# Kernel optimization log

Hardware: AMD Instinct MI355X
Metric: run time of the kernel (lower is better)

## Reference

```python
import jax, jax.numpy as jnp
import numpy as np

KERNEL = 31
GROUPS = 8
EPS = 1e-5


def mha1d(x, Wq, Wk, Wv, rel):
    """Sliding-window multi-head attention (MutliHeadAttention1D).
    x: [b, s, in_f]; Wq/Wk/Wv: [out_f, in_f] (torch Linear layout); rel: [1, out_f, KERNEL].
    Returns (out [b, s, out_f], attn [b, s, GROUPS, KERNEL])."""
    b, s, _ = x.shape
    out_f = Wq.shape[0]
    d = out_f // GROUPS
    pad = (KERNEL - 1) // 2
    xp = jnp.pad(x, ((0, 0), (pad, pad), (0, 0)))
    q = jnp.einsum('bsf,of->bso', x, Wq)          # [b, s, out_f]
    k = jnp.einsum('bsf,of->bso', xp, Wk)         # [b, s+2*pad, out_f]
    v = jnp.einsum('bsf,of->bso', xp, Wv)
    # unfold: window index [s, KERNEL]
    idx = jnp.arange(s)[:, None] + jnp.arange(KERNEL)[None, :]
    kw = jnp.swapaxes(k[:, idx], 2, 3) + rel       # [b, s, out_f, KERNEL]
    vw = jnp.swapaxes(v[:, idx], 2, 3)             # [b, s, out_f, KERNEL]
    kw = kw.reshape(b, s, GROUPS, d, KERNEL)
    vw = vw.reshape(b, s, GROUPS, d, KERNEL)
    qh = q.reshape(b, s, GROUPS, d, 1)
    energy = jnp.sum(qh * kw, axis=-2, keepdims=True)   # [b, s, g, 1, K]
    attn = jax.nn.softmax(energy, axis=-1)               # [b, s, g, 1, K]
    out = jnp.sum(attn * vw, axis=-1).reshape(b, s, out_f)
    return out, attn[:, :, :, 0, :]


def layer_norm(x, g, b):
    mu = jnp.mean(x, axis=-1, keepdims=True)
    var = jnp.mean(jnp.square(x - mu), axis=-1, keepdims=True)
    return (x - mu) / jnp.sqrt(var + EPS) * g + b


def setup_inputs() -> dict:
    key = jax.random.key(0)
    ks = jax.random.split(key, 20)
    in_f, mc, out_f = 229, 48, 88
    d = {}
    d['spec'] = jax.random.normal(ks[0], (8, 8192, in_f), dtype=jnp.float32)
    # onset attention block (in 229 -> 48)
    d['Wq1'] = jax.random.normal(ks[1], (mc, in_f), dtype=jnp.float32) * 0.1
    d['Wk1'] = jax.random.normal(ks[2], (mc, in_f), dtype=jnp.float32) * 0.1
    d['Wv1'] = jax.random.normal(ks[3], (mc, in_f), dtype=jnp.float32) * 0.1
    d['rel1'] = jax.random.normal(ks[4], (1, mc, KERNEL), dtype=jnp.float32)
    d['ln1_g'] = jnp.ones((mc,), jnp.float32)
    d['ln1_b'] = jnp.zeros((mc,), jnp.float32)
    d['Wo'] = jax.random.normal(ks[5], (out_f, mc), dtype=jnp.float32) * 0.1
    d['bo'] = jnp.zeros((out_f,), jnp.float32)
    # frame attention block (in 48+88=136 -> 48)
    in2 = mc + out_f
    d['Wq2'] = jax.random.normal(ks[6], (mc, in2), dtype=jnp.float32) * 0.1
    d['Wk2'] = jax.random.normal(ks[7], (mc, in2), dtype=jnp.float32) * 0.1
    d['Wv2'] = jax.random.normal(ks[8], (mc, in2), dtype=jnp.float32) * 0.1
    d['rel2'] = jax.random.normal(ks[9], (1, mc, KERNEL), dtype=jnp.float32)
    d['ln2_g'] = jnp.ones((mc,), jnp.float32)
    d['ln2_b'] = jnp.zeros((mc,), jnp.float32)
    d['Wf'] = jax.random.normal(ks[10], (out_f, mc), dtype=jnp.float32) * 0.1
    d['bf'] = jnp.zeros((out_f,), jnp.float32)
    return d


def reference(spec, Wq1, Wk1, Wv1, rel1, ln1_g, ln1_b, Wo, bo,
              Wq2, Wk2, Wv2, rel2, ln2_g, ln2_b, Wf, bf):
    x, a = mha1d(spec, Wq1, Wk1, Wv1, rel1)
    x = layer_norm(x, ln1_g, ln1_b)
    onset_pred = jax.nn.sigmoid(jnp.einsum('bsm,om->bso', x, Wo) + bo)
    x = jnp.concatenate((onset_pred, x), axis=-1)
    x, _ = mha1d(x, Wq2, Wk2, Wv2, rel2)
    x = layer_norm(x, ln2_g, ln2_b)
    frame_pred = jax.nn.sigmoid(jnp.einsum('bsm,om->bso', x, Wf) + bf)
    return frame_pred, onset_pred, a
```

## Files before the change

kernel.cpp:

```cpp
#include <hip/hip_runtime.h>
#include <math.h>

namespace {

constexpr int B_   = 8;
constexpr int S_   = 8192;
constexpr int NROW = B_ * S_;
constexpr int MC   = 48;
constexpr int OF   = 88;
constexpr int KW   = 31;
constexpr int F1   = 229;
constexpr int F2   = 136;

typedef __attribute__((ext_vector_type(8))) short bf16x8;
typedef __attribute__((ext_vector_type(4))) float f32x4;

__device__ inline unsigned short f2bf(float v) {
    unsigned u = __float_as_uint(v);
    unsigned r = (u + 0x7FFFu + ((u >> 16) & 1u)) >> 16;
    return (unsigned short)r;
}
__device__ inline float bf2f(unsigned short b) {
    return __uint_as_float((unsigned)b << 16);
}
__device__ inline unsigned pack2(unsigned short a, unsigned short b) {
    return (unsigned)a | ((unsigned)b << 16);
}

__global__ void wprep_kernel(const float* __restrict__ Wq,
                             const float* __restrict__ Wk,
                             const float* __restrict__ Wv,
                             int K, int nch, unsigned short* __restrict__ out) {
    int idx = blockIdx.x * 256 + threadIdx.x;
    int kpad = nch * 32;
    int total = 144 * kpad;
    if (idx >= total) return;
    int oc = idx / kpad;
    int kg = idx - oc * kpad;
    int c  = kg >> 5, kk = kg & 31;
    float val = 0.f;
    if (kg < K) {
        const float* W = (oc < 48) ? Wq : (oc < 96 ? Wk : Wv);
        int ocl = (oc < 48) ? oc : (oc < 96 ? oc - 48 : oc - 96);
        val = W[ocl * K + kg];
    }
    unsigned short h = f2bf(val);
    unsigned short l = f2bf(val - bf2f(h));
    size_t base = (size_t)c * 16384 + (size_t)oc * 56 + kk;
    out[base]        = h;
    out[base + 8192] = l;
}

__global__ void woprep_kernel(const float* __restrict__ W,
                              unsigned short* __restrict__ out) {
    int idx = blockIdx.x * 256 + threadIdx.x;
    if (idx >= 96 * 64) return;
    int n = idx >> 6, k = idx & 63;
    float val = (n < OF && k < MC) ? W[n * MC + k] : 0.f;
    unsigned short h = f2bf(val);
    unsigned short l = f2bf(val - bf2f(h));
    out[idx]        = h;
    out[6144 + idx] = l;
}

template<int K, int NCH>
__global__ __launch_bounds__(256) void proj_mfma(
    const float* __restrict__ x,
    const unsigned short* __restrict__ wbuf,
    float* __restrict__ qo, float* __restrict__ ko, float* __restrict__ vo)
{
    __shared__ __attribute__((aligned(16))) unsigned short Ah[64 * 56];
    __shared__ __attribute__((aligned(16))) unsigned short Al[64 * 56];
    __shared__ __attribute__((aligned(16))) unsigned short Bblk[16384];

    const int tid  = threadIdx.x;
    const int row0 = blockIdx.x * 64;
    const int lane = tid & 63;
    const int wm   = tid >> 6;

    f32x4 acc[9];
    #pragma unroll
    for (int nt = 0; nt < 9; ++nt) acc[nt] = f32x4{0.f, 0.f, 0.f, 0.f};

    const int arow = wm * 16 + (lane & 15);
    const int ak   = (lane >> 4) * 8;

    for (int c = 0; c < NCH; ++c) {
        {
            const uint4* src = (const uint4*)(wbuf + (size_t)c * 16384);
            uint4* dst = (uint4*)Bblk;
            #pragma unroll
            for (int i = 0; i < 8; ++i)
                dst[tid + 256 * i] = src[tid + 256 * i];
        }
        const int kc = c * 32;
        #pragma unroll
        for (int i = 0; i < 4; ++i) {
            int idx = tid + 256 * i;
            int r   = idx >> 4;
            int k2  = (idx & 15) * 2;
            int kg  = kc + k2;
            const float* xr = x + (size_t)(row0 + r) * K;
            float v0 = (kg     < K) ? xr[kg]     : 0.f;
            float v1 = (kg + 1 < K) ? xr[kg + 1] : 0.f;
            unsigned short h0 = f2bf(v0), h1 = f2bf(v1);
            unsigned short l0 = f2bf(v0 - bf2f(h0));
            unsigned short l1 = f2bf(v1 - bf2f(h1));
            *(unsigned*)&Ah[r * 56 + k2] = pack2(h0, h1);
            *(unsigned*)&Al[r * 56 + k2] = pack2(l0, l1);
        }
        __syncthreads();

        bf16x8 ah = *(const bf16x8*)&Ah[arow * 56 + ak];
        bf16x8 al = *(const bf16x8*)&Al[arow * 56 + ak];
        #pragma unroll
        for (int nt = 0; nt < 9; ++nt) {
            int bcol = nt * 16 + (lane & 15);
            bf16x8 bh = *(const bf16x8*)&Bblk[bcol * 56 + ak];
            bf16x8 bl = *(const bf16x8*)&Bblk[8192 + bcol * 56 + ak];
            acc[nt] = __builtin_amdgcn_mfma_f32_16x16x32_bf16(ah, bh, acc[nt], 0, 0, 0);
            acc[nt] = __builtin_amdgcn_mfma_f32_16x16x32_bf16(ah, bl, acc[nt], 0, 0, 0);
            acc[nt] = __builtin_amdgcn_mfma_f32_16x16x32_bf16(al, bh, acc[nt], 0, 0, 0);
        }
        __syncthreads();
    }

    const int orow = row0 + wm * 16 + ((lane >> 4) << 2);
    const int ocol = lane & 15;
    #pragma unroll
    for (int nt = 0; nt < 9; ++nt) {
        float* dst = (nt < 3) ? qo : (nt < 6 ? ko : vo);
        int oc = (nt % 3) * 16 + ocol;
        #pragma unroll
        for (int rg = 0; rg < 4; ++rg)
            dst[(size_t)(orow + rg) * MC + oc] = acc[nt][rg];
    }
}

template<bool FIRST>
__global__ __launch_bounds__(256, 4) void attn_kernel(
    const float* __restrict__ qb,
    const float* __restrict__ kb,
    const float* __restrict__ vb,
    const float* __restrict__ rel,
    const float* __restrict__ lng,
    const float* __restrict__ lnb,
    const unsigned short* __restrict__ wop,
    const float* __restrict__ bo,
    float* __restrict__ pred,
    float* __restrict__ attn_out,
    float* __restrict__ x2)
{
    __shared__ __attribute__((aligned(16))) float ks[62 * 52];
    __shared__ __attribute__((aligned(16))) float vs[62 * 52];
    __shared__ __attribute__((aligned(16))) float relT[31 * 52];
    __shared__ __attribute__((aligned(16))) unsigned short lnbuf[2][32 * 48 + 64];
    __shared__ float bosL[96];
    __shared__ float lngs[48], lnbs[48];

    const int tid  = threadIdx.x;
    const int bb   = blockIdx.x >> 8;
    const int st0  = (blockIdx.x & 255) * 32;
    const size_t base = (size_t)bb * S_;

    for (int idx = tid; idx < 744; idx += 256) {
        int rr = idx / 12, c4 = idx - rr * 12;
        int si = st0 - 15 + rr;
        float4 kv4 = {0.f, 0.f, 0.f, 0.f}, vv4 = {0.f, 0.f, 0.f, 0.f};
        if (si >= 0 && si < S_) {
            kv4 = *(const float4*)&kb[(base + si) * MC + c4 * 4];
            vv4 = *(const float4*)&vb[(base + si) * MC + c4 * 4];
        }
        *(float4*)&ks[rr * 52 + c4 * 4] = kv4;
        *(float4*)&vs[rr * 52 + c4 * 4] = vv4;
    }
    for (int idx = tid; idx < MC * KW; idx += 256) {
        int c = idx / KW, j = idx - c * KW;
        relT[j * 52 + c] = rel[idx];
    }
    if (tid < 96) bosL[tid] = (tid < OF) ? bo[tid] : 0.f;
    if (tid >= 128 && tid < 176) {
        lngs[tid - 128] = lng[tid - 128];
        lnbs[tid - 128] = lnb[tid - 128];
    }
    __syncthreads();

    const int rl  = tid >> 3;
    const int g   = tid & 7;
    const int ch0 = g * 6;
    const size_t grow = base + st0 + rl;

    const float* qr = qb + grow * MC + ch0;
    float2 q01 = *(const float2*)(qr);
    float2 q23 = *(const float2*)(qr + 2);
    float2 q45 = *(const float2*)(qr + 4);

    float e[KW];
    #pragma unroll
    for (int j = 0; j < KW; ++j) {
        const float* rp = &relT[j * 52 + ch0];
        float2 r01 = *(const float2*)(rp);
        float2 r23 = *(const float2*)(rp + 2);
        float2 r45 = *(const float2*)(rp + 4);
        e[j] = q01.x * r01.x + q01.y * r01.y + q23.x * r23.x
             + q23.y * r23.y + q45.x * r45.x + q45.y * r45.y;
    }
    float mx = -1e30f;
    #pragma unroll
    for (int j = 0; j < KW; ++j) {
        const float* kp = &ks[(rl + j) * 52 + ch0];
        float2 k01 = *(const float2*)(kp);
        float2 k23 = *(const float2*)(kp + 2);
        float2 k45 = *(const float2*)(kp + 4);
        float s = e[j] + q01.x * k01.x + q01.y * k01.y + q23.x * k23.x
                       + q23.y * k23.y + q45.x * k45.x + q45.y * k45.y;
        e[j] = s;
        mx = fmaxf(mx, s);
    }
    float den = 0.f;
    #pragma unroll
    for (int j = 0; j < KW; ++j) { float t = __expf(e[j] - mx); e[j] = t; den += t; }
    float rden = 1.f / den;

    float o0 = 0.f, o1 = 0.f, o2 = 0.f, o3 = 0.f, o4 = 0.f, o5 = 0.f;
    #pragma unroll
    for (int j = 0; j < KW; ++j) {
        float aw = e[j] * rden;
        if constexpr (FIRST) attn_out[(grow * 8 + g) * KW + j] = aw;
        const float* vp = &vs[(rl + j) * 52 + ch0];
        float2 v01 = *(const float2*)(vp);
        float2 v23 = *(const float2*)(vp + 2);
        float2 v45 = *(const float2*)(vp + 4);
        o0 += aw * v01.x; o1 += aw * v01.y; o2 += aw * v23.x;
        o3 += aw * v23.y; o4 += aw * v45.x; o5 += aw * v45.y;
    }

    float sum = o0 + o1 + o2 + o3 + o4 + o5;
    sum += __shfl_xor(sum, 1, 8);
    sum += __shfl_xor(sum, 2, 8);
    sum += __shfl_xor(sum, 4, 8);
    float mu = sum * (1.f / 48.f);
    float d0 = o0 - mu, d1 = o1 - mu, d2 = o2 - mu, d3 = o3 - mu, d4 = o4 - mu, d5 = o5 - mu;
    float vr = d0*d0 + d1*d1 + d2*d2 + d3*d3 + d4*d4 + d5*d5;
    vr += __shfl_xor(vr, 1, 8);
    vr += __shfl_xor(vr, 2, 8);
    vr += __shfl_xor(vr, 4, 8);
    float rstd = rsqrtf(vr * (1.f / 48.f) + 1e-5f);
    float y[6];
    y[0] = d0 * rstd * lngs[ch0]     + lnbs[ch0];
    y[1] = d1 * rstd * lngs[ch0 + 1] + lnbs[ch0 + 1];
    y[2] = d2 * rstd * lngs[ch0 + 2] + lnbs[ch0 + 2];
    y[3] = d3 * rstd * lngs[ch0 + 3] + lnbs[ch0 + 3];
    y[4] = d4 * rstd * lngs[ch0 + 4] + lnbs[ch0 + 4];
    y[5] = d5 * rstd * lngs[ch0 + 5] + lnbs[ch0 + 5];

    {
        unsigned short h[6], lo[6];
        #pragma unroll
        for (int c = 0; c < 6; ++c) {
            h[c]  = f2bf(y[c]);
            lo[c] = f2bf(y[c] - bf2f(h[c]));
        }
        unsigned* ph = (unsigned*)&lnbuf[0][rl * 48 + ch0];
        unsigned* pl = (unsigned*)&lnbuf[1][rl * 48 + ch0];
        ph[0] = pack2(h[0], h[1]);  ph[1] = pack2(h[2], h[3]);  ph[2] = pack2(h[4], h[5]);
        pl[0] = pack2(lo[0], lo[1]); pl[1] = pack2(lo[2], lo[3]); pl[2] = pack2(lo[4], lo[5]);
    }
    if constexpr (FIRST) {
        float* xp = x2 + grow * F2 + OF + ch0;
        *(float2*)(xp)     = float2{y[0], y[1]};
        *(float2*)(xp + 2) = float2{y[2], y[3]};
        *(float2*)(xp + 4) = float2{y[4], y[5]};
    }
    __syncthreads();

    const int l  = tid & 63;
    const int w  = tid >> 6;
    const int m  = w & 1;
    const int ng = w >> 1;
    const int lr = l & 15;
    const int lk = (l >> 4) * 8;

    bf16x8 bh[3][2], bl[3][2];
    #pragma unroll
    for (int nt = 0; nt < 3; ++nt) {
        int ncol = (ng * 3 + nt) * 16 + lr;
        #pragma unroll
        for (int kc = 0; kc < 2; ++kc) {
            size_t boff = (size_t)ncol * 64 + kc * 32 + lk;
            bh[nt][kc] = *(const bf16x8*)&wop[boff];
            bl[nt][kc] = *(const bf16x8*)&wop[6144 + boff];
        }
    }
    const int arow = m * 16 + lr;
    bf16x8 ah0 = *(const bf16x8*)&lnbuf[0][arow * 48 + lk];
    bf16x8 al0 = *(const bf16x8*)&lnbuf[1][arow * 48 + lk];
    bf16x8 ah1 = *(const bf16x8*)&lnbuf[0][arow * 48 + 32 + lk];
    bf16x8 al1 = *(const bf16x8*)&lnbuf[1][arow * 48 + 32 + lk];

    f32x4 acc[3];
    #pragma unroll
    for (int nt = 0; nt < 3; ++nt) acc[nt] = f32x4{0.f, 0.f, 0.f, 0.f};
    #pragma unroll
    for (int nt = 0; nt < 3; ++nt) {
        acc[nt] = __builtin_amdgcn_mfma_f32_16x16x32_bf16(ah0, bh[nt][0], acc[nt], 0, 0, 0);
        acc[nt] = __builtin_amdgcn_mfma_f32_16x16x32_bf16(ah0, bl[nt][0], acc[nt], 0, 0, 0);
        acc[nt] = __builtin_amdgcn_mfma_f32_16x16x32_bf16(al0, bh[nt][0], acc[nt], 0, 0, 0);
        acc[nt] = __builtin_amdgcn_mfma_f32_16x16x32_bf16(ah1, bh[nt][1], acc[nt], 0, 0, 0);
        acc[nt] = __builtin_amdgcn_mfma_f32_16x16x32_bf16(ah1, bl[nt][1], acc[nt], 0, 0, 0);
        acc[nt] = __builtin_amdgcn_mfma_f32_16x16x32_bf16(al1, bh[nt][1], acc[nt], 0, 0, 0);
    }

    const int rowo = st0 + m * 16 + ((l >> 4) << 2);
    #pragma unroll
    for (int nt = 0; nt < 3; ++nt) {
        int col = (ng * 3 + nt) * 16 + lr;
        if (col < OF) {
            float bias = bosL[col];
            #pragma unroll
            for (int rg = 0; rg < 4; ++rg) {
                float s  = acc[nt][rg] + bias;
                float sg = 1.f / (1.f + __expf(-s));
                size_t row = base + rowo + rg;
                pred[row * OF + col] = sg;
                if constexpr (FIRST) x2[row * F2 + col] = sg;
            }
        }
    }
}

}

extern "C" void kernel_launch(void* const* d_in, const int* in_sizes, int n_in,
                              void* d_out, int out_size, void* d_ws, size_t ws_size,
                              hipStream_t stream) {
    const float* spec = (const float*)d_in[0];
    const float* Wq1  = (const float*)d_in[1];
    const float* Wk1  = (const float*)d_in[2];
    const float* Wv1  = (const float*)d_in[3];
    const float* rel1 = (const float*)d_in[4];
    const float* ln1g = (const float*)d_in[5];
    const float* ln1b = (const float*)d_in[6];
    const float* Wo   = (const float*)d_in[7];
    const float* bo   = (const float*)d_in[8];
    const float* Wq2  = (const float*)d_in[9];
    const float* Wk2  = (const float*)d_in[10];
    const float* Wv2  = (const float*)d_in[11];
    const float* rel2 = (const float*)d_in[12];
    const float* ln2g = (const float*)d_in[13];
    const float* ln2b = (const float*)d_in[14];
    const float* Wf   = (const float*)d_in[15];
    const float* bf_  = (const float*)d_in[16];

    float* outf   = (float*)d_out;
    float* frame  = outf;
    float* onset  = outf + (size_t)NROW * OF;
    float* attn_a = outf + (size_t)2 * NROW * OF;

    float* wsf = (float*)d_ws;
    float* q1 = wsf;
    float* k1 = q1 + (size_t)NROW * MC;
    float* v1 = k1 + (size_t)NROW * MC;
    float* x2 = v1 + (size_t)NROW * MC;
    unsigned short* wbuf1 = (unsigned short*)(x2 + (size_t)NROW * F2);
    unsigned short* wbuf2 = wbuf1 + (size_t)8 * 16384;
    unsigned short* woP1  = wbuf2 + (size_t)5 * 16384;
    unsigned short* woP2  = woP1 + 2 * 6144;

    wprep_kernel<<<(144 * 8 * 32 + 255) / 256, 256, 0, stream>>>(Wq1, Wk1, Wv1, F1, 8, wbuf1);
    wprep_kernel<<<(144 * 5 * 32 + 255) / 256, 256, 0, stream>>>(Wq2, Wk2, Wv2, F2, 5, wbuf2);
    woprep_kernel<<<24, 256, 0, stream>>>(Wo, woP1);
    woprep_kernel<<<24, 256, 0, stream>>>(Wf, woP2);

    proj_mfma<F1, 8><<<NROW / 64, 256, 0, stream>>>(spec, wbuf1, q1, k1, v1);
    attn_kernel<true><<<NROW / 32, 256, 0, stream>>>(q1, k1, v1, rel1, ln1g, ln1b,
                                                     woP1, bo, onset, attn_a, x2);
    proj_mfma<F2, 5><<<NROW / 64, 256, 0, stream>>>(x2, wbuf2, q1, k1, v1);
    attn_kernel<false><<<NROW / 32, 256, 0, stream>>>(q1, k1, v1, rel2, ln2g, ln2b,
                                                      woP2, bf_, frame, nullptr, nullptr);
}
```

Before: 182.9 us.

## Split attention and output GEMM into separate kernels with larger attention tiles

The fused attention-plus-output-projection kernel is split in two. One kernel computes windowed attention and layernorm over 64-row tiles with 512 threads, using a blockIdx remap, and writes the normalized result to x2. A second kernel reads it back, converts it to split bf16, and runs the MFMA sigmoid projection. The aim is to cut register and LDS pressure in the attention kernel and improve halo reuse. The cost is an extra launch, an extra global round trip of the LN output, and the second pass also writing x2 during the frame stage.

```diff
diff --git a/kernel.cpp b/kernel.cpp
--- a/kernel.cpp
+++ b/kernel.cpp
@@ -138,51 +138,43 @@
 }
 
 template<bool FIRST>
-__global__ __launch_bounds__(256, 4) void attn_kernel(
+__global__ __launch_bounds__(512, 8) void attn_core(
     const float* __restrict__ qb,
     const float* __restrict__ kb,
     const float* __restrict__ vb,
     const float* __restrict__ rel,
     const float* __restrict__ lng,
     const float* __restrict__ lnb,
-    const unsigned short* __restrict__ wop,
-    const float* __restrict__ bo,
-    float* __restrict__ pred,
     float* __restrict__ attn_out,
     float* __restrict__ x2)
 {
-    __shared__ __attribute__((aligned(16))) float ks[62 * 52];
-    __shared__ __attribute__((aligned(16))) float vs[62 * 52];
+    __shared__ __attribute__((aligned(16))) float ks[94 * 52];
+    __shared__ __attribute__((aligned(16))) float vs[94 * 52];
     __shared__ __attribute__((aligned(16))) float relT[31 * 52];
-    __shared__ __attribute__((aligned(16))) unsigned short lnbuf[2][32 * 48 + 64];
-    __shared__ float bosL[96];
     __shared__ float lngs[48], lnbs[48];
 
-    const int tid  = threadIdx.x;
-    const int bb   = blockIdx.x >> 8;
-    const int st0  = (blockIdx.x & 255) * 32;
+    const int tid = threadIdx.x;
+    const int bid = ((blockIdx.x & 7) << 7) | (blockIdx.x >> 3);
+    const int bb  = bid >> 7;
+    const int st0 = (bid & 127) * 64;
     const size_t base = (size_t)bb * S_;
 
-    for (int idx = tid; idx < 744; idx += 256) {
+    for (int idx = tid; idx < 94 * 12; idx += 512) {
         int rr = idx / 12, c4 = idx - rr * 12;
         int si = st0 - 15 + rr;
-        float4 kv4 = {0.f, 0.f, 0.f, 0.f}, vv4 = {0.f, 0.f, 0.f, 0.f};
+        float4 k4 = {0.f, 0.f, 0.f, 0.f}, v4 = {0.f, 0.f, 0.f, 0.f};
         if (si >= 0 && si < S_) {
-            kv4 = *(const float4*)&kb[(base + si) * MC + c4 * 4];
-            vv4 = *(const float4*)&vb[(base + si) * MC + c4 * 4];
-        }
-        *(float4*)&ks[rr * 52 + c4 * 4] = kv4;
-        *(float4*)&vs[rr * 52 + c4 * 4] = vv4;
-    }
-    for (int idx = tid; idx < MC * KW; idx += 256) {
+            k4 = *(const float4*)&kb[(base + si) * MC + c4 * 4];
+            v4 = *(const float4*)&vb[(base + si) * MC + c4 * 4];
+        }
+        *(float4*)&ks[rr * 52 + c4 * 4] = k4;
+        *(float4*)&vs[rr * 52 + c4 * 4] = v4;
+    }
+    for (int idx = tid; idx < MC * KW; idx += 512) {
         int c = idx / KW, j = idx - c * KW;
         relT[j * 52 + c] = rel[idx];
     }
-    if (tid < 96) bosL[tid] = (tid < OF) ? bo[tid] : 0.f;
-    if (tid >= 128 && tid < 176) {
-        lngs[tid - 128] = lng[tid - 128];
-        lnbs[tid - 128] = lnb[tid - 128];
-    }
+    if (tid < 48) { lngs[tid] = lng[tid]; lnbs[tid] = lnb[tid]; }
     __syncthreads();
 
     const int rl  = tid >> 3;
@@ -223,10 +215,11 @@
     float rden = 1.f / den;
 
     float o0 = 0.f, o1 = 0.f, o2 = 0.f, o3 = 0.f, o4 = 0.f, o5 = 0.f;
+    float* aout = FIRST ? (attn_out + (grow * 8 + g) * KW) : nullptr;
     #pragma unroll
     for (int j = 0; j < KW; ++j) {
         float aw = e[j] * rden;
-        if constexpr (FIRST) attn_out[(grow * 8 + g) * KW + j] = aw;
+        if constexpr (FIRST) aout[j] = aw;
         const float* vp = &vs[(rl + j) * 52 + ch0];
         float2 v01 = *(const float2*)(vp);
         float2 v23 = *(const float2*)(vp + 2);
@@ -246,84 +239,83 @@
     vr += __shfl_xor(vr, 2, 8);
     vr += __shfl_xor(vr, 4, 8);
     float rstd = rsqrtf(vr * (1.f / 48.f) + 1e-5f);
-    float y[6];
-    y[0] = d0 * rstd * lngs[ch0]     + lnbs[ch0];
-    y[1] = d1 * rstd * lngs[ch0 + 1] + lnbs[ch0 + 1];
-    y[2] = d2 * rstd * lngs[ch0 + 2] + lnbs[ch0 + 2];
-    y[3] = d3 * rstd * lngs[ch0 + 3] + lnbs[ch0 + 3];
-    y[4] = d4 * rstd * lngs[ch0 + 4] + lnbs[ch0 + 4];
-    y[5] = d5 * rstd * lngs[ch0 + 5] + lnbs[ch0 + 5];
-
-    {
-        unsigned short h[6], lo[6];
-        #pragma unroll
-        for (int c = 0; c < 6; ++c) {
-            h[c]  = f2bf(y[c]);
-            lo[c] = f2bf(y[c] - bf2f(h[c]));
-        }
-        unsigned* ph = (unsigned*)&lnbuf[0][rl * 48 + ch0];
-        unsigned* pl = (unsigned*)&lnbuf[1][rl * 48 + ch0];
-        ph[0] = pack2(h[0], h[1]);  ph[1] = pack2(h[2], h[3]);  ph[2] = pack2(h[4], h[5]);
-        pl[0] = pack2(lo[0], lo[1]); pl[1] = pack2(lo[2], lo[3]); pl[2] = pack2(lo[4], lo[5]);
-    }
-    if constexpr (FIRST) {
-        float* xp = x2 + grow * F2 + OF + ch0;
-        *(float2*)(xp)     = float2{y[0], y[1]};
-        *(float2*)(xp + 2) = float2{y[2], y[3]};
-        *(float2*)(xp + 4) = float2{y[4], y[5]};
-    }
+
+    float* xp = x2 + grow * F2 + OF + ch0;
+    *(float2*)(xp)     = float2{d0 * rstd * lngs[ch0]     + lnbs[ch0],
+                                d1 * rstd * lngs[ch0 + 1] + lnbs[ch0 + 1]};
+    *(float2*)(xp + 2) = float2{d2 * rstd * lngs[ch0 + 2] + lnbs[ch0 + 2],
+                                d3 * rstd * lngs[ch0 + 3] + lnbs[ch0 + 3]};
+    *(float2*)(xp + 4) = float2{d4 * rstd * lngs[ch0 + 4] + lnbs[ch0 + 4],
+                                d5 * rstd * lngs[ch0 + 5] + lnbs[ch0 + 5]};
+}
+
+template<bool FIRST>
+__global__ __launch_bounds__(256) void pred_gemm(
+    const float* __restrict__ x2,
+    const unsigned short* __restrict__ wop,
+    const float* __restrict__ bo,
+    float* __restrict__ pred,
+    float* __restrict__ x2w)
+{
+    __shared__ __attribute__((aligned(16))) unsigned short yh[64 * 72];
+    __shared__ __attribute__((aligned(16))) unsigned short yl[64 * 72];
+    __shared__ float bosL[96];
+
+    const int tid  = threadIdx.x;
+    const int row0 = blockIdx.x * 64;
+
+    for (int idx = tid; idx < 768; idx += 256) {
+        int r = idx / 12, c4 = idx - r * 12;
+        float4 v4 = *(const float4*)&x2[(size_t)(row0 + r) * F2 + OF + c4 * 4];
+        unsigned short h0 = f2bf(v4.x), h1 = f2bf(v4.y), h2 = f2bf(v4.z), h3 = f2bf(v4.w);
+        unsigned short l0 = f2bf(v4.x - bf2f(h0)), l1 = f2bf(v4.y - bf2f(h1));
+        unsigned short l2 = f2bf(v4.z - bf2f(h2)), l3 = f2bf(v4.w - bf2f(h3));
+        *(uint2*)&yh[r * 72 + c4 * 4] = uint2{pack2(h0, h1), pack2(h2, h3)};
+        *(uint2*)&yl[r * 72 + c4 * 4] = uint2{pack2(l0, l1), pack2(l2, l3)};
+    }
+    for (int idx = tid; idx < 384; idx += 256) {
+        int r = idx / 6, u = idx - r * 6;
+        *(uint2*)&yh[r * 72 + 48 + u * 4] = uint2{0u, 0u};
+        *(uint2*)&yl[r * 72 + 48 + u * 4] = uint2{0u, 0u};
+    }
+    if (tid < 96) bosL[tid] = (tid < OF) ? bo[tid] : 0.f;
     __syncthreads();
 
-    const int l  = tid & 63;
-    const int w  = tid >> 6;
-    const int m  = w & 1;
-    const int ng = w >> 1;
-    const int lr = l & 15;
-    const int lk = (l >> 4) * 8;
-
-    bf16x8 bh[3][2], bl[3][2];
-    #pragma unroll
-    for (int nt = 0; nt < 3; ++nt) {
-        int ncol = (ng * 3 + nt) * 16 + lr;
-        #pragma unroll
-        for (int kc = 0; kc < 2; ++kc) {
-            size_t boff = (size_t)ncol * 64 + kc * 32 + lk;
-            bh[nt][kc] = *(const bf16x8*)&wop[boff];
-            bl[nt][kc] = *(const bf16x8*)&wop[6144 + boff];
-        }
-    }
-    const int arow = m * 16 + lr;
-    bf16x8 ah0 = *(const bf16x8*)&lnbuf[0][arow * 48 + lk];
-    bf16x8 al0 = *(const bf16x8*)&lnbuf[1][arow * 48 + lk];
-    bf16x8 ah1 = *(const bf16x8*)&lnbuf[0][arow * 48 + 32 + lk];
-    bf16x8 al1 = *(const bf16x8*)&lnbuf[1][arow * 48 + 32 + lk];
-
-    f32x4 acc[3];
-    #pragma unroll
-    for (int nt = 0; nt < 3; ++nt) acc[nt] = f32x4{0.f, 0.f, 0.f, 0.f};
-    #pragma unroll
-    for (int nt = 0; nt < 3; ++nt) {
-        acc[nt] = __builtin_amdgcn_mfma_f32_16x16x32_bf16(ah0, bh[nt][0], acc[nt], 0, 0, 0);
-        acc[nt] = __builtin_amdgcn_mfma_f32_16x16x32_bf16(ah0, bl[nt][0], acc[nt], 0, 0, 0);
-        acc[nt] = __builtin_amdgcn_mfma_f32_16x16x32_bf16(al0, bh[nt][0], acc[nt], 0, 0, 0);
-        acc[nt] = __builtin_amdgcn_mfma_f32_16x16x32_bf16(ah1, bh[nt][1], acc[nt], 0, 0, 0);
-        acc[nt] = __builtin_amdgcn_mfma_f32_16x16x32_bf16(ah1, bl[nt][1], acc[nt], 0, 0, 0);
-        acc[nt] = __builtin_amdgcn_mfma_f32_16x16x32_bf16(al1, bh[nt][1], acc[nt], 0, 0, 0);
-    }
-
-    const int rowo = st0 + m * 16 + ((l >> 4) << 2);
-    #pragma unroll
-    for (int nt = 0; nt < 3; ++nt) {
-        int col = (ng * 3 + nt) * 16 + lr;
-        if (col < OF) {
-            float bias = bosL[col];
+    const int l   = tid & 63;
+    const int w   = tid >> 6;
+    const int lr  = l & 15;
+    const int lk8 = (l >> 4) * 8;
+
+    const int arow = w * 16 + lr;
+    bf16x8 ah0 = *(const bf16x8*)&yh[arow * 72 + lk8];
+    bf16x8 al0 = *(const bf16x8*)&yl[arow * 72 + lk8];
+    bf16x8 ah1 = *(const bf16x8*)&yh[arow * 72 + 32 + lk8];
+    bf16x8 al1 = *(const bf16x8*)&yl[arow * 72 + 32 + lk8];
+
+    const int rowo = row0 + w * 16 + ((l >> 4) << 2);
+    #pragma unroll
+    for (int nt = 0; nt < 6; ++nt) {
+        int ncol = nt * 16 + lr;
+        bf16x8 bh0 = *(const bf16x8*)&wop[(size_t)ncol * 64 + lk8];
+        bf16x8 bl0 = *(const bf16x8*)&wop[6144 + (size_t)ncol * 64 + lk8];
+        bf16x8 bh1 = *(const bf16x8*)&wop[(size_t)ncol * 64 + 32 + lk8];
+        bf16x8 bl1 = *(const bf16x8*)&wop[6144 + (size_t)ncol * 64 + 32 + lk8];
+        f32x4 oacc = f32x4{0.f, 0.f, 0.f, 0.f};
+        oacc = __builtin_amdgcn_mfma_f32_16x16x32_bf16(ah0, bh0, oacc, 0, 0, 0);
+        oacc = __builtin_amdgcn_mfma_f32_16x16x32_bf16(ah0, bl0, oacc, 0, 0, 0);
+        oacc = __builtin_amdgcn_mfma_f32_16x16x32_bf16(al0, bh0, oacc, 0, 0, 0);
+        oacc = __builtin_amdgcn_mfma_f32_16x16x32_bf16(ah1, bh1, oacc, 0, 0, 0);
+        oacc = __builtin_amdgcn_mfma_f32_16x16x32_bf16(ah1, bl1, oacc, 0, 0, 0);
+        oacc = __builtin_amdgcn_mfma_f32_16x16x32_bf16(al1, bh1, oacc, 0, 0, 0);
+        if (ncol < OF) {
+            float bias = bosL[ncol];
             #pragma unroll
             for (int rg = 0; rg < 4; ++rg) {
-                float s  = acc[nt][rg] + bias;
+                float s  = oacc[rg] + bias;
                 float sg = 1.f / (1.f + __expf(-s));
-                size_t row = base + rowo + rg;
-                pred[row * OF + col] = sg;
-                if constexpr (FIRST) x2[row * F2 + col] = sg;
+                size_t row = (size_t)(rowo + rg);
+                pred[row * OF + ncol] = sg;
+                if constexpr (FIRST) x2w[row * F2 + ncol] = sg;
             }
         }
     }
@@ -373,9 +365,11 @@
     woprep_kernel<<<24, 256, 0, stream>>>(Wf, woP2);
 
     proj_mfma<F1, 8><<<NROW / 64, 256, 0, stream>>>(spec, wbuf1, q1, k1, v1);
-    attn_kernel<true><<<NROW / 32, 256, 0, stream>>>(q1, k1, v1, rel1, ln1g, ln1b,
-                                                     woP1, bo, onset, attn_a, x2);
+    attn_core<true><<<NROW / 64, 512, 0, stream>>>(q1, k1, v1, rel1, ln1g, ln1b,
+                                                   attn_a, x2);
+    pred_gemm<true><<<NROW / 64, 256, 0, stream>>>(x2, woP1, bo, onset, x2);
     proj_mfma<F2, 5><<<NROW / 64, 256, 0, stream>>>(x2, wbuf2, q1, k1, v1);
-    attn_kernel<false><<<NROW / 32, 256, 0, stream>>>(q1, k1, v1, rel2, ln2g, ln2b,
-                                                      woP2, bf_, frame, nullptr, nullptr);
-}
+    attn_core<false><<<NROW / 64, 512, 0, stream>>>(q1, k1, v1, rel2, ln2g, ln2b,
+                                                    nullptr, x2);
+    pred_gemm<false><<<NROW / 64, 256, 0, stream>>>(x2, woP2, bf_, frame, nullptr);
+}
```

Result: slower. 203.5 us (+11.2%).
